# Optimization experiments

Hardware: AMD Instinct MI355X
Metric: run time of the kernel (lower is better)

## Reference

```python
import jax, jax.numpy as jnp
from jax import lax
import numpy as np

WS = 8      # window size
NH = 16     # num heads
DIM = 256   # channels
BN_EPS = 1e-5


def _rel_index(ws):
    # Swin-style relative position index, shape [ws*ws, ws*ws], static int
    coords = np.stack(np.meshgrid(np.arange(ws), np.arange(ws), indexing='ij')).reshape(2, -1)
    rel = coords[:, :, None] - coords[:, None, :]
    return (rel[0] + ws - 1) * (2 * ws - 1) + (rel[1] + ws - 1)


def _conv(x, w, pad, groups=1):
    return lax.conv_general_dilated(x, w, (1, 1), pad,
                                    dimension_numbers=('NCHW', 'OIHW', 'NCHW'),
                                    feature_group_count=groups)


def setup_inputs() -> dict:
    key = jax.random.key(0)
    ks = jax.random.split(key, 13)
    C = DIM
    s = 0.05
    return {
        'x': jax.random.normal(ks[0], (2, C, 256, 256), jnp.float32),
        'w_qkv': jax.random.normal(ks[1], (3 * C, C), jnp.float32) * s,
        'rel_table': jax.random.normal(ks[2], ((2 * WS - 1) ** 2, NH), jnp.float32) * 0.02,
        'w_attnx': jax.random.normal(ks[3], (C, C, WS, 1), jnp.float32) * s,
        'b_attnx': jax.random.normal(ks[4], (C,), jnp.float32) * s,
        'w_attny': jax.random.normal(ks[5], (C, C, 1, WS), jnp.float32) * s,
        'b_attny': jax.random.normal(ks[6], (C,), jnp.float32) * s,
        'w_dw': jax.random.normal(ks[7], (C, 1, WS, WS), jnp.float32) * s,
        'bn_gamma': jax.random.uniform(ks[8], (C,), jnp.float32) + 0.5,
        'bn_beta': jax.random.normal(ks[9], (C,), jnp.float32) * s,
        'bn_mean': jax.random.normal(ks[10], (C,), jnp.float32) * s,
        'bn_var': jax.random.uniform(ks[11], (C,), jnp.float32) + 0.5,
        'w_proj': jax.random.normal(ks[12], (C, C), jnp.float32) * s,
    }


def reference(x, w_qkv, rel_table, w_attnx, b_attnx, w_attny, b_attny,
              w_dw, bn_gamma, bn_beta, bn_mean, bn_var, w_proj):
    B, C, H, W = x.shape
    ws, nh = WS, NH
    d = C // nh
    scale = d ** -0.5
    hh, ww = H // ws, W // ws  # H, W divisible by ws -> pad() is a no-op

    # qkv 1x1 conv (no bias)
    qkv = jnp.einsum('bchw,oc->bohw', x, w_qkv)  # [B, 3C, H, W]
    # b (qkv h d) (hh ws1) (ww ws2) -> qkv (b hh ww) h (ws1 ws2) d
    qkv = qkv.reshape(B, 3, nh, d, hh, ws, ww, ws).transpose(1, 0, 4, 6, 2, 5, 7, 3)
    qkv = qkv.reshape(3, B * hh * ww, nh, ws * ws, d)
    q, k, v = qkv[0], qkv[1], qkv[2]

    dots = jnp.einsum('nhid,nhjd->nhij', q, k) * scale  # [N, h, 64, 64]
    idx = _rel_index(ws).reshape(-1)
    bias = rel_table[idx].reshape(ws * ws, ws * ws, nh).transpose(2, 0, 1)  # [h, 64, 64]
    attn = jax.nn.softmax(dots + bias[None], axis=-1)
    o = jnp.einsum('nhij,nhjd->nhid', attn, v)
    # (b hh ww) h (ws1 ws2) d -> b (h d) (hh ws1) (ww ws2)
    o = o.reshape(B, hh, ww, nh, ws, ws, d).transpose(0, 3, 6, 1, 4, 2, 5).reshape(B, C, H, W)

    p = ws // 2 - 1  # 3
    ox = _conv(jnp.pad(o, ((0, 0), (0, 0), (0, 1), (0, 0)), 'reflect'), w_attnx,
               [(p, p), (0, 0)]) + b_attnx[None, :, None, None]
    oy = _conv(jnp.pad(o, ((0, 0), (0, 0), (0, 0), (0, 1)), 'reflect'), w_attny,
               [(0, 0), (p, p)]) + b_attny[None, :, None, None]
    out = ox + oy

    # pad_out + SeparableConvBN(depthwise ws x ws, BN eval, 1x1)
    out = jnp.pad(out, ((0, 0), (0, 0), (0, 1), (0, 1)), 'reflect')
    pd = (ws - 1) // 2  # 3
    out = _conv(out, w_dw, [(pd, pd), (pd, pd)], groups=C)
    out = (out - bn_mean[None, :, None, None]) / jnp.sqrt(bn_var[None, :, None, None] + BN_EPS)
    out = out * bn_gamma[None, :, None, None] + bn_beta[None, :, None, None]
    out = jnp.einsum('bchw,oc->bohw', out, w_proj)
    return out[:, :, :H, :W]
```

## Files before the change

kernel.cpp:

```cpp
#include <hip/hip_runtime.h>
#include <stdint.h>


#define B_ 2
#define C_ 256
#define H_ 256
#define W_ 256
#define HW_ 65536

typedef unsigned short u16;
typedef unsigned int u32;
typedef short bf16x8 __attribute__((ext_vector_type(8)));
typedef float f32x4 __attribute__((ext_vector_type(4)));
typedef float f32x16 __attribute__((ext_vector_type(16)));

__device__ __forceinline__ float b2f(u16 h) {
  union { u32 u; float f; } x; x.u = ((u32)h) << 16; return x.f;
}
__device__ __forceinline__ float b2f_lo(u32 u) {
  union { u32 v; float f; } x; x.v = u << 16; return x.f;
}
__device__ __forceinline__ float b2f_hi(u32 u) {
  union { u32 v; float f; } x; x.v = u & 0xffff0000u; return x.f;
}
__device__ __forceinline__ u16 f2b(float f) {
  union { float f; u32 u; } x; x.f = f;
  return (u16)((x.u + 0x7fffu + ((x.u >> 16) & 1u)) >> 16);
}
__device__ __forceinline__ u32 pack2(float a, float b) {
  return (u32)f2b(a) | ((u32)f2b(b) << 16);
}
__device__ __forceinline__ u32 pack2rn(float a, float b) {
  u32 ua = __float_as_uint(a) + 0x8000u;
  u32 ub = __float_as_uint(b) + 0x8000u;
  return __builtin_amdgcn_perm(ub, ua, 0x07060302u);
}
__device__ __forceinline__ u16 f2brn(float f) {
  return (u16)((__float_as_uint(f) + 0x8000u) >> 16);
}

__global__ __launch_bounds__(256) void k_wt(
    const float* __restrict__ wx, const float* __restrict__ wy,
    const float* __restrict__ wqkv, const float* __restrict__ rel,
    u16* __restrict__ wt, float* __restrict__ biasT)
{
  const int o = blockIdx.x, c = threadIdx.x;
  const float* px = wx + ((size_t)o * 256 + c) * 8;
  const float* py = wy + ((size_t)o * 256 + c) * 8;
#pragma unroll
  for (int t = 0; t < 8; ++t) {
    wt[(size_t)t * 65536 + o * 256 + c]          = f2b(px[t]);
    wt[524288 + (size_t)t * 65536 + o * 256 + c] = f2b(py[t]);
  }
  u16* w8 = wt + 1048576;
#pragma unroll
  for (int t = 0; t < 3; ++t) {
    const int row = o + t * 256;
    w8[(size_t)row * 256 + c] = f2b(wqkv[(size_t)row * 256 + c]);
  }
  const int flat = o * 256 + c;
  const int h = flat >> 12, j = (flat >> 6) & 63, i = flat & 63;
  const int iy = i >> 3, ix = i & 7, jy = j >> 3, jx = j & 7;
  const int ridx = (iy - jy + 7) * 15 + (ix - jx + 7);
  biasT[flat] = rel[ridx * 16 + h];
}

__global__ __launch_bounds__(256) void k_attn(
    const float* __restrict__ x, const u16* __restrict__ w8,
    const float* __restrict__ biasT, u16* __restrict__ o_img)
{
  __shared__ __align__(16) union {
    u16 xb[64][264];
    u16 P[4][4096];
  } U;
  __shared__ __align__(16) u16 q_s[64][264];
  __shared__ __align__(16) u16 k_s[64][264];
  __shared__ __align__(16) u16 v_sT[256][72];

  const int tid = threadIdx.x;
  const int nb  = blockIdx.x;
  const int b   = nb >> 10;
  const int hh  = (nb >> 5) & 31;
  const int ww  = nb & 31;
  const int h0  = hh << 3, w0 = ww << 3;

  {
    const int c2 = tid & 127;
    const int half = tid >> 7;
    const float* p0 = x + (((size_t)(b * C_ + 2 * c2)) * H_ + (h0 + half * 4)) * W_ + w0;
    const float* p1 = p0 + (size_t)H_ * W_;
#pragma unroll
    for (int r = 0; r < 4; ++r) {
      const float4 a0 = *(const float4*)(p0 + r * W_);
      const float4 a1 = *(const float4*)(p0 + r * W_ + 4);
      const float4 b0 = *(const float4*)(p1 + r * W_);
      const float4 b1 = *(const float4*)(p1 + r * W_ + 4);
      const float fa[8] = {a0.x, a0.y, a0.z, a0.w, a1.x, a1.y, a1.z, a1.w};
      const float fb[8] = {b0.x, b0.y, b0.z, b0.w, b1.x, b1.y, b1.z, b1.w};
      const int px0 = (half * 4 + r) * 8;
#pragma unroll
      for (int cc = 0; cc < 8; ++cc)
        *(u32*)&U.xb[px0 + cc][2 * c2] = pack2rn(fa[cc], fb[cc]);
    }
  }
  __syncthreads();

  const int lane = tid & 63, wid = tid >> 6;
  const int n = lane & 31, h5 = lane >> 5;

  f32x16 acc[6][2];
#pragma unroll
  for (int mt = 0; mt < 6; ++mt)
#pragma unroll
    for (int nt = 0; nt < 2; ++nt)
#pragma unroll
      for (int i = 0; i < 16; ++i) acc[mt][nt][i] = 0.f;

#pragma unroll 2
  for (int kb = 0; kb < 16; ++kb) {
    const int k0 = kb * 16;
    bf16x8 bfr[2];
#pragma unroll
    for (int nt = 0; nt < 2; ++nt) {
      union { uint4 u; bf16x8 v; } T;
      T.u = *(const uint4*)&U.xb[nt * 32 + n][k0 + h5 * 8];
      bfr[nt] = T.v;
    }
#pragma unroll
    for (int mt = 0; mt < 6; ++mt) {
      const int row = (mt >> 1) * 256 + wid * 64 + (mt & 1) * 32 + n;
      union { uint4 u; bf16x8 v; } A;
      A.u = *(const uint4*)(w8 + (size_t)row * 256 + k0 + h5 * 8);
      acc[mt][0] = __builtin_amdgcn_mfma_f32_32x32x16_bf16(A.v, bfr[0], acc[mt][0], 0, 0, 0);
      acc[mt][1] = __builtin_amdgcn_mfma_f32_32x32x16_bf16(A.v, bfr[1], acc[mt][1], 0, 0, 0);
    }
  }

  const int chb0 = wid * 64 + 4 * h5;
#pragma unroll
  for (int mt = 0; mt < 4; ++mt) {
    u16 (*dst)[264] = (mt < 2) ? q_s : k_s;
    const float qs = (mt < 2) ? 0.25f : 1.0f;
    const int chb = chb0 + (mt & 1) * 32;
#pragma unroll
    for (int nt = 0; nt < 2; ++nt) {
      const int px = nt * 32 + n;
#pragma unroll
      for (int m = 0; m < 8; ++m) {
        const int ch = chb + ((2 * m) & 3) + 8 * (m >> 1);
        *(u32*)&dst[px][ch] =
            pack2rn(acc[mt][nt][2 * m] * qs, acc[mt][nt][2 * m + 1] * qs);
      }
    }
  }
#pragma unroll
  for (int mt = 4; mt < 6; ++mt) {
    const int chb = chb0 + (mt & 1) * 32;
#pragma unroll
    for (int nt = 0; nt < 2; ++nt) {
      const int px = nt * 32 + n;
#pragma unroll
      for (int r = 0; r < 16; ++r) {
        const int ch = chb + (r & 3) + 8 * (r >> 2);
        v_sT[ch][px] = f2brn(acc[mt][nt][r]);
      }
    }
  }
  __syncthreads();

  u16* Pw = U.P[wid];
  const int il = lane & 15, jg = lane >> 4;

  for (int hl = 0; hl < 4; ++hl) {
    const int head = wid * 4 + hl;
    const int hb = head * 16;

    bf16x8 ak[2], bq[2];
#pragma unroll
    for (int jt = 0; jt < 2; ++jt) {
      union { uint4 u; bf16x8 v; } T;
      T.u = *(const uint4*)&k_s[jt * 32 + n][hb + h5 * 8];
      ak[jt] = T.v;
    }
#pragma unroll
    for (int it = 0; it < 2; ++it) {
      union { uint4 u; bf16x8 v; } T;
      T.u = *(const uint4*)&q_s[it * 32 + n][hb + h5 * 8];
      bq[it] = T.v;
    }
    f32x16 zro;
#pragma unroll
    for (int e = 0; e < 16; ++e) zro[e] = 0.f;
    f32x16 s[2][2];
#pragma unroll
    for (int jt = 0; jt < 2; ++jt)
#pragma unroll
      for (int it = 0; it < 2; ++it)
        s[jt][it] = __builtin_amdgcn_mfma_f32_32x32x16_bf16(ak[jt], bq[it], zro, 0, 0, 0);

    const float* bT = biasT + head * 4096;
#pragma unroll
    for (int jt = 0; jt < 2; ++jt)
#pragma unroll
      for (int it = 0; it < 2; ++it)
#pragma unroll
        for (int r = 0; r < 16; ++r) {
          const int j = jt * 32 + (r & 3) + 8 * (r >> 2) + 4 * h5;
          s[jt][it][r] += bT[j * 64 + it * 32 + n];
        }

#pragma unroll
    for (int it = 0; it < 2; ++it) {
      const int i = it * 32 + n;
      float mx = s[0][it][0];
#pragma unroll
      for (int jt = 0; jt < 2; ++jt)
#pragma unroll
        for (int r = 0; r < 16; ++r) mx = fmaxf(mx, s[jt][it][r]);
      mx = fmaxf(mx, __shfl_xor(mx, 32));
      float sum = 0.f;
#pragma unroll
      for (int jt = 0; jt < 2; ++jt)
#pragma unroll
        for (int r = 0; r < 16; ++r) {
          const float p = __expf(s[jt][it][r] - mx);
          s[jt][it][r] = p;
          sum += p;
        }
      sum += __shfl_xor(sum, 32);
      const float rs = 1.0f / sum;
      const u32 rowoff = (u32)(i * 128);
      const u32 swz = (u32)((i & 7) << 4);
#pragma unroll
      for (int jt = 0; jt < 2; ++jt)
#pragma unroll
        for (int m = 0; m < 8; ++m) {
          const int j = jt * 32 + ((2 * m) & 3) + 8 * (m >> 1) + 4 * h5;
          const u32 off = (rowoff + (u32)(j * 2)) ^ swz;
          *(u32*)((char*)Pw + off) =
              pack2rn(s[jt][it][2 * m] * rs, s[jt][it][2 * m + 1] * rs);
        }
    }

    bf16x8 bv[2];
#pragma unroll
    for (int ks = 0; ks < 2; ++ks) {
      union { uint4 u; bf16x8 v; } T;
      T.u = *(const uint4*)&v_sT[hb + il][ks * 32 + jg * 8];
      bv[ks] = T.v;
    }
#pragma unroll
    for (int it2 = 0; it2 < 4; ++it2) {
      f32x4 pv = {0.f, 0.f, 0.f, 0.f};
#pragma unroll
      for (int ks = 0; ks < 2; ++ks) {
        const int i = it2 * 16 + il;
        const u32 off =
            ((u32)(i * 128 + ks * 64 + jg * 16)) ^ ((u32)((i & 7) << 4));
        union { uint4 u; bf16x8 v; } A;
        A.u = *(const uint4*)((const char*)Pw + off);
        pv = __builtin_amdgcn_mfma_f32_16x16x32_bf16(A.v, bv[ks], pv, 0, 0, 0);
      }
#pragma unroll
      for (int rr = 0; rr < 4; ++rr) {
        const int i = it2 * 16 + jg * 4 + rr;
        const int iy = i >> 3, ix = i & 7;
        o_img[(((size_t)(b * H_ + h0 + iy)) * W_ + (w0 + ix)) * C_ + hb + il] =
            f2brn(pv[rr]);
      }
    }
  }
}

__global__ __launch_bounds__(256, 2) void k_conv2m(
    const u16* __restrict__ o_nhwc, const u16* __restrict__ wt,
    const float* __restrict__ bxg, const float* __restrict__ byg,
    u16* __restrict__ out1)
{
  __shared__ u16 tile[9 * 136 * 20];
  __shared__ float bias_l[128];

  const int tid = threadIdx.x;
  const int nb = (blockIdx.x & 7) * 128 + (blockIdx.x >> 3);
  const int wh = nb & 1, oh = (nb >> 1) & 1, hg = (nb >> 2) & 127, b = nb >> 9;
  const int h0 = hg << 1;
  const int ob = oh * 128, wb0 = wh * 128;
  const int lane = tid & 63, wid = tid >> 6;
  const int o64 = (wid & 1) * 64;
  const int w64 = ((wid >> 1) & 1) * 64;
  const int n = lane & 31, h5 = lane >> 5;

  if (tid < 128) bias_l[tid] = bxg[ob + tid] + byg[ob + tid];

  const u16* srcp[5];
  u32 dstoff[5];
#pragma unroll
  for (int k = 0; k < 5; ++k) {
    const int e = tid + (k << 8);
    srcp[k] = nullptr;
    dstoff[k] = 0;
    if (e < 1224) {
      const int r = e / 136, wi = e - r * 136;
      const int hp = h0 - 3 + r;
      const int wp = wb0 + wi - 4;
      dstoff[k] = (u32)((r * 136 + wi) * 20);
      if (hp >= 0 && hp <= 256 && wp >= 0 && wp <= 256) {
        const int hr = (hp == 256) ? 254 : hp;
        const int wr = (wp == 256) ? 254 : wp;
        srcp[k] = o_nhwc + (((size_t)(b * H_ + hr)) * W_ + wr) * C_;
      }
    }
  }

  uint4 pre[5][2];
#pragma unroll
  for (int k = 0; k < 5; ++k) {
    pre[k][0] = make_uint4(0, 0, 0, 0);
    pre[k][1] = make_uint4(0, 0, 0, 0);
    if (srcp[k]) {
      pre[k][0] = *(const uint4*)(srcp[k]);
      pre[k][1] = *(const uint4*)(srcp[k] + 8);
    }
  }

  f32x16 acc[2][2][2];
#pragma unroll
  for (int r2 = 0; r2 < 2; ++r2)
#pragma unroll
    for (int mt = 0; mt < 2; ++mt)
#pragma unroll
      for (int nt = 0; nt < 2; ++nt)
#pragma unroll
        for (int i = 0; i < 16; ++i) acc[r2][mt][nt][i] = 0.f;

  for (int cb = 0; cb < 16; ++cb) {
    const int c0 = cb * 16;
    __syncthreads();
#pragma unroll
    for (int k = 0; k < 5; ++k) {
      if (tid + (k << 8) < 1224) {
        u16* d = &tile[dstoff[k]];
        *(uint2*)(d)      = make_uint2(pre[k][0].x, pre[k][0].y);
        *(uint2*)(d + 4)  = make_uint2(pre[k][0].z, pre[k][0].w);
        *(uint2*)(d + 8)  = make_uint2(pre[k][1].x, pre[k][1].y);
        *(uint2*)(d + 12) = make_uint2(pre[k][1].z, pre[k][1].w);
      }
    }
    __syncthreads();
    if (cb < 15) {
      const int c1 = c0 + 16;
#pragma unroll
      for (int k = 0; k < 5; ++k) {
        pre[k][0] = make_uint4(0, 0, 0, 0);
        pre[k][1] = make_uint4(0, 0, 0, 0);
        if (srcp[k]) {
          pre[k][0] = *(const uint4*)(srcp[k] + c1);
          pre[k][1] = *(const uint4*)(srcp[k] + c1 + 8);
        }
      }
    }
#pragma unroll
    for (int cv = 0; cv < 2; ++cv) {
      const u16* wbase = wt + (size_t)cv * 524288;
#pragma unroll
      for (int t = 0; t < 8; ++t) {
        bf16x8 a[2];
#pragma unroll
        for (int mt = 0; mt < 2; ++mt) {
          const int o = ob + o64 + mt * 32 + n;
          union { uint4 u; bf16x8 v; } Uu;
          Uu.u = *(const uint4*)(wbase + ((size_t)(t * 256 + o)) * 256 + c0 + h5 * 8);
          a[mt] = Uu.v;
        }
        bf16x8 bb[2][2];
#pragma unroll
        for (int r2 = 0; r2 < 2; ++r2)
#pragma unroll
          for (int nt = 0; nt < 2; ++nt) {
            const int rr = cv ? (r2 + 3) : (r2 + t);
            const int wi = w64 + nt * 32 + n + (cv ? (t + 1) : 4);
            const u16* p = &tile[(rr * 136 + wi) * 20 + h5 * 8];
            union { uint2 u[2]; bf16x8 v; } Uu;
            Uu.u[0] = *(const uint2*)p;
            Uu.u[1] = *(const uint2*)(p + 4);
            bb[r2][nt] = Uu.v;
          }
#pragma unroll
        for (int r2 = 0; r2 < 2; ++r2) {
          acc[r2][0][0] = __builtin_amdgcn_mfma_f32_32x32x16_bf16(a[0], bb[r2][0], acc[r2][0][0], 0, 0, 0);
          acc[r2][0][1] = __builtin_amdgcn_mfma_f32_32x32x16_bf16(a[0], bb[r2][1], acc[r2][0][1], 0, 0, 0);
          acc[r2][1][0] = __builtin_amdgcn_mfma_f32_32x32x16_bf16(a[1], bb[r2][0], acc[r2][1][0], 0, 0, 0);
          acc[r2][1][1] = __builtin_amdgcn_mfma_f32_32x32x16_bf16(a[1], bb[r2][1], acc[r2][1][1], 0, 0, 0);
        }
      }
    }
  }
#pragma unroll
  for (int r2 = 0; r2 < 2; ++r2)
#pragma unroll
    for (int mt = 0; mt < 2; ++mt)
#pragma unroll
      for (int nt = 0; nt < 2; ++nt)
#pragma unroll
        for (int r = 0; r < 16; ++r) {
          const int om = o64 + mt * 32 + (r & 3) + 8 * (r >> 2) + 4 * h5;
          const int o = ob + om;
          const int wg = wb0 + w64 + nt * 32 + n;
          const float v = acc[r2][mt][nt][r] + bias_l[om];
          out1[(((size_t)(b * C_ + o)) * H_ + (h0 + r2)) * W_ + wg] = f2b(v);
        }
}

__global__ __launch_bounds__(256) void k_dwbn(
    const u16* __restrict__ out1, const float* __restrict__ wdw,
    const float* __restrict__ gam, const float* __restrict__ bet,
    const float* __restrict__ mea, const float* __restrict__ var,
    u16* __restrict__ bno)
{
  __shared__ u16 tile[23][264];
  const int tid = threadIdx.x, nb = blockIdx.x;
  const int c = nb & 255, ht = (nb >> 8) & 15, b = nb >> 12;
  const int h0 = ht * 16;

  for (int e = tid; e < 23 * 264; e += 256) {
    const int tr = e / 264, tc = e % 264;
    const int r = h0 - 3 + tr;
    const int cg = tc - 3;
    u16 v = 0;
    if (r >= 0 && r <= 256 && cg >= 0 && cg <= 256) {
      const int rr = (r == 256) ? 254 : r;
      const int cgm = (cg == 256) ? 254 : cg;
      v = out1[(((size_t)(b * C_ + c)) * H_ + rr) * W_ + cgm];
    }
    tile[tr][tc] = v;
  }
  float wk[64];
#pragma unroll
  for (int k2 = 0; k2 < 64; ++k2) wk[k2] = wdw[c * 64 + k2];
  const float scl = gam[c] / sqrtf(var[c] + 1e-5f);
  const float shf = bet[c] - mea[c] * scl;
  __syncthreads();

  const int wg = tid & 31, hg = tid >> 5;
  const int w0 = wg * 8;
#pragma unroll
  for (int k = 0; k < 2; ++k) {
    const int hl = hg * 2 + k;
    float a[8];
#pragma unroll
    for (int s = 0; s < 8; ++s) a[s] = 0.f;
#pragma unroll
    for (int i = 0; i < 8; ++i) {
      const uint4 va = *(const uint4*)&tile[hl + i][w0];
      const uint4 vb = *(const uint4*)&tile[hl + i][w0 + 8];
      float f[16];
      f[0] = b2f_lo(va.x);  f[1] = b2f_hi(va.x);  f[2] = b2f_lo(va.y);  f[3] = b2f_hi(va.y);
      f[4] = b2f_lo(va.z);  f[5] = b2f_hi(va.z);  f[6] = b2f_lo(va.w);  f[7] = b2f_hi(va.w);
      f[8] = b2f_lo(vb.x);  f[9] = b2f_hi(vb.x);  f[10] = b2f_lo(vb.y); f[11] = b2f_hi(vb.y);
      f[12] = b2f_lo(vb.z); f[13] = b2f_hi(vb.z); f[14] = b2f_lo(vb.w); f[15] = b2f_hi(vb.w);
#pragma unroll
      for (int j = 0; j < 8; ++j) {
        const float wv = wk[i * 8 + j];
#pragma unroll
        for (int s = 0; s < 8; ++s) a[s] += f[s + j] * wv;
      }
    }
    uint4 uv;
    uv.x = pack2(a[0] * scl + shf, a[1] * scl + shf);
    uv.y = pack2(a[2] * scl + shf, a[3] * scl + shf);
    uv.z = pack2(a[4] * scl + shf, a[5] * scl + shf);
    uv.w = pack2(a[6] * scl + shf, a[7] * scl + shf);
    *(uint4*)&bno[(((size_t)(b * C_ + c)) * H_ + h0 + hl) * W_ + w0] = uv;
  }
}

__global__ __launch_bounds__(256) void k_projm(
    const u16* __restrict__ bn, const float* __restrict__ wp, float* __restrict__ out)
{
  const int tid = threadIdx.x, nb = blockIdx.x;
  const int oh = nb & 1;
  const int pb = nb >> 1;
  const int b  = pb >> 9;
  const int px0 = (pb & 511) << 7;
  const int lane = tid & 63, wid = tid >> 6;
  const int wo = (wid >> 1) * 64, wpx = (wid & 1) * 64;
  const int n = lane & 31, h5 = lane >> 5;
  const int ob = oh * 128;
  const int pxl = px0 + wpx + n;

  f32x16 acc[2][2];
#pragma unroll
  for (int mt = 0; mt < 2; ++mt)
#pragma unroll
    for (int nt = 0; nt < 2; ++nt)
#pragma unroll
      for (int i = 0; i < 16; ++i) acc[mt][nt][i] = 0.f;

  const u16* bnb = bn + (size_t)b * C_ * HW_;
#pragma unroll 2
  for (int cb = 0; cb < 16; ++cb) {
    const int c0 = cb * 16;
    bf16x8 a[2];
#pragma unroll
    for (int mt = 0; mt < 2; ++mt) {
      const int row = ob + wo + mt * 32 + n;
      const float4 w0v = *(const float4*)&wp[(size_t)row * 256 + c0 + h5 * 8];
      const float4 w1v = *(const float4*)&wp[(size_t)row * 256 + c0 + h5 * 8 + 4];
      union { u32 u[4]; bf16x8 v; } T;
      T.u[0] = pack2rn(w0v.x, w0v.y);
      T.u[1] = pack2rn(w0v.z, w0v.w);
      T.u[2] = pack2rn(w1v.x, w1v.y);
      T.u[3] = pack2rn(w1v.z, w1v.w);
      a[mt] = T.v;
    }
    bf16x8 bb[2];
#pragma unroll
    for (int nt = 0; nt < 2; ++nt) {
      const u16* sp = bnb + (size_t)(c0 + h5 * 8) * HW_ + (pxl + nt * 32);
      const u32 e0 = sp[0 * HW_], e1 = sp[1 * HW_], e2 = sp[2 * HW_], e3 = sp[3 * HW_];
      const u32 e4 = sp[4 * HW_], e5 = sp[5 * HW_], e6 = sp[6 * HW_], e7 = sp[7 * HW_];
      union { u32 u[4]; bf16x8 v; } T;
      T.u[0] = e0 | (e1 << 16);
      T.u[1] = e2 | (e3 << 16);
      T.u[2] = e4 | (e5 << 16);
      T.u[3] = e6 | (e7 << 16);
      bb[nt] = T.v;
    }
    acc[0][0] = __builtin_amdgcn_mfma_f32_32x32x16_bf16(a[0], bb[0], acc[0][0], 0, 0, 0);
    acc[0][1] = __builtin_amdgcn_mfma_f32_32x32x16_bf16(a[0], bb[1], acc[0][1], 0, 0, 0);
    acc[1][0] = __builtin_amdgcn_mfma_f32_32x32x16_bf16(a[1], bb[0], acc[1][0], 0, 0, 0);
    acc[1][1] = __builtin_amdgcn_mfma_f32_32x32x16_bf16(a[1], bb[1], acc[1][1], 0, 0, 0);
  }
#pragma unroll
  for (int mt = 0; mt < 2; ++mt)
#pragma unroll
    for (int nt = 0; nt < 2; ++nt)
#pragma unroll
      for (int r = 0; r < 16; ++r) {
        const int o = ob + wo + mt * 32 + (r & 3) + 8 * (r >> 2) + 4 * h5;
        out[((size_t)(b * C_ + o)) * HW_ + (pxl + nt * 32)] = acc[mt][nt][r];
      }
}

extern "C" void kernel_launch(void* const* d_in, const int* in_sizes, int n_in,
                              void* d_out, int out_size, void* d_ws, size_t ws_size,
                              hipStream_t stream)
{
  const float* x     = (const float*)d_in[0];
  const float* wqkv  = (const float*)d_in[1];
  const float* rel   = (const float*)d_in[2];
  const float* wax   = (const float*)d_in[3];
  const float* bax   = (const float*)d_in[4];
  const float* way   = (const float*)d_in[5];
  const float* bay   = (const float*)d_in[6];
  const float* wdw   = (const float*)d_in[7];
  const float* gam   = (const float*)d_in[8];
  const float* bet   = (const float*)d_in[9];
  const float* mea   = (const float*)d_in[10];
  const float* var   = (const float*)d_in[11];
  const float* wproj = (const float*)d_in[12];
  float* out = (float*)d_out;

  const size_t N = (size_t)B_ * C_ * H_ * W_;
  u16* oNHWC  = (u16*)d_out;
  u16* out1b  = (u16*)d_out + N;
  u16* wtbuf  = (u16*)d_ws;
  float* biasT = (float*)((char*)d_ws + 2490368);
  u16* bnbuf  = (u16*)d_ws;

  hipLaunchKernelGGL(k_wt,     dim3(256),  dim3(256), 0, stream, wax, way, wqkv, rel, wtbuf, biasT);
  hipLaunchKernelGGL(k_attn,   dim3(2048), dim3(256), 0, stream, x, wtbuf + 1048576, biasT, oNHWC);
  hipLaunchKernelGGL(k_conv2m, dim3(1024), dim3(256), 0, stream, oNHWC, wtbuf, bax, bay, out1b);
  hipLaunchKernelGGL(k_dwbn,   dim3(8192), dim3(256), 0, stream, out1b, wdw, gam, bet, mea, var, bnbuf);
  hipLaunchKernelGGL(k_projm,  dim3(2048), dim3(256), 0, stream, bnbuf, wproj, out);
}
```

Measured before the change: 979.8 us.

## Drop register prefetch and shrink LDS tile pitch to fit three blocks per CU

The conv2m kernel stops prefetching the next channel slice into registers. It now loads each slice straight from global memory before writing it into the shared-memory tile. The tile row pitch drops from 20 to 18 elements and the launch bound rises to three blocks per CU, so the aim is higher occupancy from fewer registers and less LDS. The trade-off is that global loads are no longer overlapped with MFMA work within a block. The 36-byte pitch also leaves the 8-byte LDS accesses misaligned, which may split them or change bank-conflict behaviour.

```diff
diff --git a/kernel.cpp b/kernel.cpp
--- a/kernel.cpp
+++ b/kernel.cpp
@@ -272,12 +272,12 @@
   }
 }
 
-__global__ __launch_bounds__(256, 2) void k_conv2m(
+__global__ __launch_bounds__(256, 3) void k_conv2m(
     const u16* __restrict__ o_nhwc, const u16* __restrict__ wt,
     const float* __restrict__ bxg, const float* __restrict__ byg,
     u16* __restrict__ out1)
 {
-  __shared__ u16 tile[9 * 136 * 20];
+  __shared__ u16 tile[9 * 136 * 18];
   __shared__ float bias_l[128];
 
   const int tid = threadIdx.x;
@@ -303,7 +303,7 @@
       const int r = e / 136, wi = e - r * 136;
       const int hp = h0 - 3 + r;
       const int wp = wb0 + wi - 4;
-      dstoff[k] = (u32)((r * 136 + wi) * 20);
+      dstoff[k] = (u32)((r * 136 + wi) * 18);
       if (hp >= 0 && hp <= 256 && wp >= 0 && wp <= 256) {
         const int hr = (hp == 256) ? 254 : hp;
         const int wr = (wp == 256) ? 254 : wp;
@@ -312,17 +312,6 @@
     }
   }
 
-  uint4 pre[5][2];
-#pragma unroll
-  for (int k = 0; k < 5; ++k) {
-    pre[k][0] = make_uint4(0, 0, 0, 0);
-    pre[k][1] = make_uint4(0, 0, 0, 0);
-    if (srcp[k]) {
-      pre[k][0] = *(const uint4*)(srcp[k]);
-      pre[k][1] = *(const uint4*)(srcp[k] + 8);
-    }
-  }
-
   f32x16 acc[2][2][2];
 #pragma unroll
   for (int r2 = 0; r2 < 2; ++r2)
@@ -339,26 +328,19 @@
 #pragma unroll
     for (int k = 0; k < 5; ++k) {
       if (tid + (k << 8) < 1224) {
+        uint4 A = make_uint4(0, 0, 0, 0), Bv = A;
+        if (srcp[k]) {
+          A  = *(const uint4*)(srcp[k] + c0);
+          Bv = *(const uint4*)(srcp[k] + c0 + 8);
+        }
         u16* d = &tile[dstoff[k]];
-        *(uint2*)(d)      = make_uint2(pre[k][0].x, pre[k][0].y);
-        *(uint2*)(d + 4)  = make_uint2(pre[k][0].z, pre[k][0].w);
-        *(uint2*)(d + 8)  = make_uint2(pre[k][1].x, pre[k][1].y);
-        *(uint2*)(d + 12) = make_uint2(pre[k][1].z, pre[k][1].w);
+        *(uint2*)(d)      = make_uint2(A.x, A.y);
+        *(uint2*)(d + 4)  = make_uint2(A.z, A.w);
+        *(uint2*)(d + 8)  = make_uint2(Bv.x, Bv.y);
+        *(uint2*)(d + 12) = make_uint2(Bv.z, Bv.w);
       }
     }
     __syncthreads();
-    if (cb < 15) {
-      const int c1 = c0 + 16;
-#pragma unroll
-      for (int k = 0; k < 5; ++k) {
-        pre[k][0] = make_uint4(0, 0, 0, 0);
-        pre[k][1] = make_uint4(0, 0, 0, 0);
-        if (srcp[k]) {
-          pre[k][0] = *(const uint4*)(srcp[k] + c1);
-          pre[k][1] = *(const uint4*)(srcp[k] + c1 + 8);
-        }
-      }
-    }
 #pragma unroll
     for (int cv = 0; cv < 2; ++cv) {
       const u16* wbase = wt + (size_t)cv * 524288;
@@ -379,7 +361,7 @@
           for (int nt = 0; nt < 2; ++nt) {
             const int rr = cv ? (r2 + 3) : (r2 + t);
             const int wi = w64 + nt * 32 + n + (cv ? (t + 1) : 4);
-            const u16* p = &tile[(rr * 136 + wi) * 20 + h5 * 8];
+            const u16* p = &tile[(rr * 136 + wi) * 18 + h5 * 8];
             union { uint2 u[2]; bf16x8 v; } Uu;
             Uu.u[0] = *(const uint2*)p;
             Uu.u[1] = *(const uint2*)(p + 4);
```

After: 1.449 ms. 1.48x slower.
